# Performance work log

Measured on AMD Instinct MI355X. Metric: run time of the kernel, lower is better.

The kernel has to match this reference:

```python
import jax, jax.numpy as jnp
import numpy as np

B, N, F_IN, H, F = 2, 2048, 128, 8, 32  # FH = 256, a has 2F = 64


def setup_inputs() -> dict:
    key = jax.random.key(0)
    k_g, k_x, k_w, k_a = jax.random.split(key, 4)
    # sparse-ish adjacency with self loops (float mask, as in the keras code)
    u = jax.random.uniform(k_g, (B, N, N), dtype=jnp.float32)
    g = jnp.maximum((u < 0.05).astype(jnp.float32), jnp.eye(N, dtype=jnp.float32)[None])
    x = jax.random.normal(k_x, (B, N, F_IN), dtype=jnp.float32)
    w = jax.random.normal(k_w, (F_IN, F * H), dtype=jnp.float32) * (1.0 / np.sqrt(F_IN))
    a = jax.random.normal(k_a, (2 * F,), dtype=jnp.float32) * 0.1
    return {"g": g, "x": x, "w": w, "a": a, "n_heads": H}


def reference(g, x, w, a, n_heads):
    # g: [B,N,N] adjacency, x: [B,N,F_in], w: [F_in, F*H], a: [2F]
    Bd, Nd, _ = g.shape
    Fh = w.shape[1] // n_heads
    # linear transform + split heads: xh[b,n,h,f] == (x@w)[b,n, f + Fh*h]
    xh = jnp.dot(x, w).reshape(Bd, Nd, n_heads, Fh)  # [B,N,H,F]
    a1, a2 = a[:Fh], a[Fh:]
    # concat-attention is linear: score[b,i,j,h] = a1.x_j + a2.x_i
    s_j = jnp.einsum('bnhf,f->bnh', xh, a1)  # contribution of the tiled-over-axis1 copy (_x1 -> node j)
    s_i = jnp.einsum('bnhf,f->bnh', xh, a2)  # contribution of _x2 -> node i
    scores = s_i[:, :, None, :] + s_j[:, None, :, :]  # [B,N,N,H]
    e = jnp.exp(jax.nn.leaky_relu(scores, negative_slope=0.2))
    # normalize by sum over neighbors j masked by adjacency (keepdims like K.sum(..., keepdims=True))
    norm = jnp.sum(e * g[..., None], axis=2, keepdims=True)  # [B,N,1,H]
    return e / norm
```

## Files before the change

### kernel.cpp

```cpp
#include <hip/hip_runtime.h>

constexpr int Bv  = 2;
constexpr int Nv  = 2048;
constexpr int FIN = 128;
constexpr int Hn  = 8;
constexpr int Fv  = 32;
constexpr int NROW = Bv * Nv;
constexpr int S    = NROW * Hn;

typedef float v4f __attribute__((ext_vector_type(4)));

__global__ __launch_bounds__(256) void prep_kernel(
    const float* __restrict__ w, const float* __restrict__ a,
    const float* __restrict__ x, float* __restrict__ pq) {
    __shared__ float wa[2 * FIN * Hn];
    const int tid = threadIdx.x;

    for (int e = tid; e < 2 * FIN * Hn; e += 256) {
        const int which = e >> 10;
        const int k     = (e >> 3) & (FIN - 1);
        const int h     = e & (Hn - 1);
        const float* ap = a + which * Fv;
        const float* wp = w + (size_t)k * (Fv * Hn) + h * Fv;
        float s = 0.f;
        #pragma unroll
        for (int f = 0; f < Fv; ++f) s = fmaf(wp[f], ap[f], s);
        wa[e] = s;
    }
    __syncthreads();

    const int row = blockIdx.x * 32 + (tid >> 3);
    const int h   = tid & (Hn - 1);
    const float* xr = x + (size_t)row * FIN;
    float sj = 0.f, si = 0.f;
    #pragma unroll 4
    for (int k = 0; k < FIN; ++k) {
        const float xv = xr[k];
        sj = fmaf(xv, wa[k * Hn + h], sj);
        si = fmaf(xv, wa[FIN * Hn + k * Hn + h], si);
    }
    const int idx = row * Hn + h;
    pq[idx]         = __expf(sj);
    pq[S + idx]     = __expf(0.2f * sj);
    pq[2 * S + idx] = __expf(si);
    pq[3 * S + idx] = __expf(0.2f * si);
}

__global__ __launch_bounds__(256) void norm_kernel(
    const float* __restrict__ g, const float* __restrict__ pq,
    float* __restrict__ tbl) {
    const int row  = blockIdx.x;
    const int b    = row >> 11;
    const int tid  = threadIdx.x;
    const int lane = tid & 63, wv = tid >> 6;

    __shared__ int   idxs[Nv];
    __shared__ int   wavesum[4];
    __shared__ int   base_s;
    __shared__ float red[4][Hn];

    if (tid == 0) base_s = 0;
    __syncthreads();

    const float* __restrict__ grow = g + (size_t)row * Nv;

    for (int c = 0; c < Nv / 256; ++c) {
        const int j = c * 256 + tid;
        const bool pred = grow[j] != 0.f;
        const unsigned long long m = __ballot(pred);
        if (lane == 0) wavesum[wv] = __popcll(m);
        __syncthreads();
        int woff = base_s;
        #pragma unroll
        for (int w2 = 0; w2 < 4; ++w2) if (w2 < wv) woff += wavesum[w2];
        const int total = wavesum[0] + wavesum[1] + wavesum[2] + wavesum[3];
        if (pred)
            idxs[woff + __popcll(m & ((1ull << lane) - 1))] = j;
        __syncthreads();
        if (tid == 0) base_s += total;
    }
    __syncthreads();
    const int cnt = base_s;

    float pi[Hn], qi[Hn];
    #pragma unroll
    for (int h = 0; h < Hn; ++h) {
        pi[h] = pq[2 * S + row * Hn + h];
        qi[h] = pq[3 * S + row * Hn + h];
    }
    const float4* __restrict__ Pj4 = (const float4*)(pq + (size_t)b * Nv * Hn);
    const float4* __restrict__ Qj4 = (const float4*)(pq + S + (size_t)b * Nv * Hn);

    float acc[Hn];
    #pragma unroll
    for (int h = 0; h < Hn; ++h) acc[h] = 0.f;

    for (int t = tid; t < cnt; t += 256) {
        const int jj = idxs[t];
        const float4 p0 = Pj4[2 * jj], p1 = Pj4[2 * jj + 1];
        const float4 q0 = Qj4[2 * jj], q1 = Qj4[2 * jj + 1];
        acc[0] += fmaxf(pi[0] * p0.x, qi[0] * q0.x);
        acc[1] += fmaxf(pi[1] * p0.y, qi[1] * q0.y);
        acc[2] += fmaxf(pi[2] * p0.z, qi[2] * q0.z);
        acc[3] += fmaxf(pi[3] * p0.w, qi[3] * q0.w);
        acc[4] += fmaxf(pi[4] * p1.x, qi[4] * q1.x);
        acc[5] += fmaxf(pi[5] * p1.y, qi[5] * q1.y);
        acc[6] += fmaxf(pi[6] * p1.z, qi[6] * q1.z);
        acc[7] += fmaxf(pi[7] * p1.w, qi[7] * q1.w);
    }

    #pragma unroll
    for (int h = 0; h < Hn; ++h) {
        float v = acc[h];
        #pragma unroll
        for (int off = 32; off > 0; off >>= 1) v += __shfl_down(v, off);
        if (lane == 0) red[wv][h] = v;
    }
    __syncthreads();
    if (tid < Hn) {
        const float nsum = red[0][tid] + red[1][tid] + red[2][tid] + red[3][tid];
        const float rn = 1.0f / nsum;
        const float piv = pq[2 * S + row * Hn + tid];
        const float qiv = pq[3 * S + row * Hn + tid];
        tbl[row * 16 + tid]     = piv * rn;
        tbl[row * 16 + 8 + tid] = qiv * rn;
    }
}

__global__ __launch_bounds__(256) void out_kernel(
    const float* __restrict__ pq, const float* __restrict__ tbl,
    float* __restrict__ out) {
    const int bid  = blockIdx.x;
    const int row  = bid >> 1;
    const int half = bid & 1;
    const int b    = row >> 11;
    const int tid  = threadIdx.x;
    const int hh   = tid & 1;

    const float4 prv = *(const float4*)(tbl + row * 16 + hh * 4);
    const float4 qrv = *(const float4*)(tbl + row * 16 + 8 + hh * 4);

    const float4* __restrict__ Pb = (const float4*)(pq + (size_t)b * Nv * Hn);
    const float4* __restrict__ Qb = (const float4*)(pq + S + (size_t)b * Nv * Hn);
    float* __restrict__ orow = out + (size_t)row * Nv * Hn;

    const int base = half * 2048 + tid;
    #pragma unroll
    for (int it = 0; it < 8; ++it) {
        const int s = base + it * 256;
        const float4 pj = Pb[s];
        const float4 qj = Qb[s];
        v4f o;
        o.x = fmaxf(prv.x * pj.x, qrv.x * qj.x);
        o.y = fmaxf(prv.y * pj.y, qrv.y * qj.y);
        o.z = fmaxf(prv.z * pj.z, qrv.z * qj.z);
        o.w = fmaxf(prv.w * pj.w, qrv.w * qj.w);
        __builtin_nontemporal_store(o, (v4f*)(orow + (size_t)s * 4));
    }
}

extern "C" void kernel_launch(void* const* d_in, const int* in_sizes, int n_in,
                              void* d_out, int out_size, void* d_ws, size_t ws_size,
                              hipStream_t stream) {
    const float* g = (const float*)d_in[0];
    const float* x = (const float*)d_in[1];
    const float* w = (const float*)d_in[2];
    const float* a = (const float*)d_in[3];

    float* pq  = (float*)d_ws;
    float* tbl = pq + 4 * S;
    float* out = (float*)d_out;

    prep_kernel<<<NROW / 32, 256, 0, stream>>>(w, a, x, pq);
    norm_kernel<<<NROW, 256, 0, stream>>>(g, pq, tbl);
    out_kernel<<<NROW * 2, 256, 0, stream>>>(pq, tbl, out);
}
```

Baseline: 87.88 us.

## Fuse norm and output kernels, vectorize adjacency compaction with float4 ballots

Merges the normalization and output-writing kernels into one per-row kernel, so the per-row scale factors stay in shared memory instead of going through a global table and an extra launch. The adjacency row scan now loads float4 and issues four ballots per iteration, which cuts the barrier-separated compaction rounds from eight to two. Output stores switch from nontemporal to regular stores, and each block now writes the whole row, so there are half as many output blocks and each does twice the work.

```diff
diff --git a/kernel.cpp b/kernel.cpp
--- a/kernel.cpp
+++ b/kernel.cpp
@@ -7,8 +7,6 @@
 constexpr int Fv  = 32;
 constexpr int NROW = Bv * Nv;
 constexpr int S    = NROW * Hn;
-
-typedef float v4f __attribute__((ext_vector_type(4)));
 
 __global__ __launch_bounds__(256) void prep_kernel(
     const float* __restrict__ w, const float* __restrict__ a,
@@ -46,9 +44,9 @@
     pq[3 * S + idx] = __expf(0.2f * si);
 }
 
-__global__ __launch_bounds__(256) void norm_kernel(
+__global__ __launch_bounds__(256) void norm_out_kernel(
     const float* __restrict__ g, const float* __restrict__ pq,
-    float* __restrict__ tbl) {
+    float* __restrict__ out) {
     const int row  = blockIdx.x;
     const int b    = row >> 11;
     const int tid  = threadIdx.x;
@@ -58,24 +56,35 @@
     __shared__ int   wavesum[4];
     __shared__ int   base_s;
     __shared__ float red[4][Hn];
+    __shared__ float pr_s[Hn], qr_s[Hn];
 
     if (tid == 0) base_s = 0;
-    __syncthreads();
 
-    const float* __restrict__ grow = g + (size_t)row * Nv;
+    const float4* __restrict__ g4 = (const float4*)(g + (size_t)row * Nv);
 
-    for (int c = 0; c < Nv / 256; ++c) {
-        const int j = c * 256 + tid;
-        const bool pred = grow[j] != 0.f;
-        const unsigned long long m = __ballot(pred);
-        if (lane == 0) wavesum[wv] = __popcll(m);
+    #pragma unroll
+    for (int it = 0; it < 2; ++it) {
+        const int q  = it * 256 + tid;
+        const float4 gv = g4[q];
+        const int j0 = q * 4;
+        const unsigned long long m0 = __ballot(gv.x != 0.f);
+        const unsigned long long m1 = __ballot(gv.y != 0.f);
+        const unsigned long long m2 = __ballot(gv.z != 0.f);
+        const unsigned long long m3 = __ballot(gv.w != 0.f);
+        if (lane == 0)
+            wavesum[wv] = __popcll(m0) + __popcll(m1) + __popcll(m2) + __popcll(m3);
         __syncthreads();
-        int woff = base_s;
+        int base = base_s;
         #pragma unroll
-        for (int w2 = 0; w2 < 4; ++w2) if (w2 < wv) woff += wavesum[w2];
+        for (int w2 = 0; w2 < 4; ++w2) if (w2 < wv) base += wavesum[w2];
         const int total = wavesum[0] + wavesum[1] + wavesum[2] + wavesum[3];
-        if (pred)
-            idxs[woff + __popcll(m & ((1ull << lane) - 1))] = j;
+        const unsigned long long below = (1ull << lane) - 1ull;
+        int off = base + __popcll(m0 & below) + __popcll(m1 & below)
+                       + __popcll(m2 & below) + __popcll(m3 & below);
+        if (gv.x != 0.f) idxs[off++] = j0;
+        if (gv.y != 0.f) idxs[off++] = j0 + 1;
+        if (gv.z != 0.f) idxs[off++] = j0 + 2;
+        if (gv.w != 0.f) idxs[off++] = j0 + 3;
         __syncthreads();
         if (tid == 0) base_s += total;
     }
@@ -120,42 +129,26 @@
     if (tid < Hn) {
         const float nsum = red[0][tid] + red[1][tid] + red[2][tid] + red[3][tid];
         const float rn = 1.0f / nsum;
-        const float piv = pq[2 * S + row * Hn + tid];
-        const float qiv = pq[3 * S + row * Hn + tid];
-        tbl[row * 16 + tid]     = piv * rn;
-        tbl[row * 16 + 8 + tid] = qiv * rn;
+        pr_s[tid] = pq[2 * S + row * Hn + tid] * rn;
+        qr_s[tid] = pq[3 * S + row * Hn + tid] * rn;
     }
-}
+    __syncthreads();
 
-__global__ __launch_bounds__(256) void out_kernel(
-    const float* __restrict__ pq, const float* __restrict__ tbl,
-    float* __restrict__ out) {
-    const int bid  = blockIdx.x;
-    const int row  = bid >> 1;
-    const int half = bid & 1;
-    const int b    = row >> 11;
-    const int tid  = threadIdx.x;
-    const int hh   = tid & 1;
+    const int hh = tid & 1;
+    const float4 pr = *(const float4*)(&pr_s[hh * 4]);
+    const float4 qr = *(const float4*)(&qr_s[hh * 4]);
 
-    const float4 prv = *(const float4*)(tbl + row * 16 + hh * 4);
-    const float4 qrv = *(const float4*)(tbl + row * 16 + 8 + hh * 4);
-
-    const float4* __restrict__ Pb = (const float4*)(pq + (size_t)b * Nv * Hn);
-    const float4* __restrict__ Qb = (const float4*)(pq + S + (size_t)b * Nv * Hn);
-    float* __restrict__ orow = out + (size_t)row * Nv * Hn;
-
-    const int base = half * 2048 + tid;
-    #pragma unroll
-    for (int it = 0; it < 8; ++it) {
-        const int s = base + it * 256;
-        const float4 pj = Pb[s];
-        const float4 qj = Qb[s];
-        v4f o;
-        o.x = fmaxf(prv.x * pj.x, qrv.x * qj.x);
-        o.y = fmaxf(prv.y * pj.y, qrv.y * qj.y);
-        o.z = fmaxf(prv.z * pj.z, qrv.z * qj.z);
-        o.w = fmaxf(prv.w * pj.w, qrv.w * qj.w);
-        __builtin_nontemporal_store(o, (v4f*)(orow + (size_t)s * 4));
+    float4* __restrict__ orow = (float4*)(out + (size_t)row * Nv * Hn);
+    #pragma unroll 4
+    for (int s = tid; s < 2 * Nv; s += 256) {
+        const float4 pj = Pj4[s];
+        const float4 qj = Qj4[s];
+        float4 o;
+        o.x = fmaxf(pr.x * pj.x, qr.x * qj.x);
+        o.y = fmaxf(pr.y * pj.y, qr.y * qj.y);
+        o.z = fmaxf(pr.z * pj.z, qr.z * qj.z);
+        o.w = fmaxf(pr.w * pj.w, qr.w * qj.w);
+        orow[s] = o;
     }
 }
 
@@ -168,10 +161,8 @@
     const float* a = (const float*)d_in[3];
 
     float* pq  = (float*)d_ws;
-    float* tbl = pq + 4 * S;
     float* out = (float*)d_out;
 
     prep_kernel<<<NROW / 32, 256, 0, stream>>>(w, a, x, pq);
-    norm_kernel<<<NROW, 256, 0, stream>>>(g, pq, tbl);
-    out_kernel<<<NROW * 2, 256, 0, stream>>>(pq, tbl, out);
+    norm_out_kernel<<<NROW, 256, 0, stream>>>(g, pq, out);
 }
```

New measurement: 96.37 us. 1.1x slower.
